# Kernel tuning notes

Hardware: AMD Instinct MI355X
Metric: run time of the kernel (lower is better)

Reference implementation:

```python
import jax, jax.numpy as jnp
import numpy as np

C = 256
NH = 4  # attention heads
G = 8   # groupnorm groups
EPS = 1e-5


def group_norm(x, weight, bias):
    B, Cc, H, W = x.shape
    xg = x.reshape(B, G, Cc // G, H, W)
    mean = xg.mean(axis=(2, 3, 4), keepdims=True)
    var = xg.var(axis=(2, 3, 4), keepdims=True)
    xg = (xg - mean) * jax.lax.rsqrt(var + EPS)
    xn = xg.reshape(B, Cc, H, W)
    return xn * weight[None, :, None, None] + bias[None, :, None, None]


def setup_inputs() -> dict:
    key = jax.random.key(0)
    ks = jax.random.split(key, 7)
    B, H, W = 16, 32, 32
    x = jax.random.normal(ks[0], (B, C, H, W), dtype=jnp.float32)
    n_weight = jnp.ones((C,), dtype=jnp.float32)
    n_bias = jnp.zeros((C,), dtype=jnp.float32)
    qkv_w = jax.random.normal(ks[1], (3 * C, C), dtype=jnp.float32) * (C ** -0.5)
    qkv_b = jnp.zeros((3 * C,), dtype=jnp.float32)
    p_w = jax.random.normal(ks[2], (C, C), dtype=jnp.float32) * (C ** -0.5)
    p_b = jnp.zeros((C,), dtype=jnp.float32)
    return {"x": x, "n_weight": n_weight, "n_bias": n_bias,
            "qkv_w": qkv_w, "qkv_b": qkv_b, "p_w": p_w, "p_b": p_b}


def reference(x, n_weight, n_bias, qkv_w, qkv_b, p_w, p_b):
    B, Cc, H, W = x.shape
    N = H * W
    dh = Cc // NH
    sc = dh ** -0.5
    xn = group_norm(x, n_weight, n_bias)  # [B,C,H,W]
    xn_flat = xn.reshape(B, Cc, N)
    # 1x1 conv == channel matmul
    qkv = jnp.einsum('oc,bcn->bon', qkv_w, xn_flat) + qkv_b[None, :, None]
    qkv = qkv.reshape(B, 3, NH, dh, N)
    q, k, v = qkv[:, 0], qkv[:, 1], qkv[:, 2]  # [B,h,dh,N]
    a = jax.nn.softmax(jnp.einsum('bhci,bhcj->bhij', q, k) * sc, axis=-1)
    o = jnp.einsum('bhij,bhcj->bhci', a, v).reshape(B, Cc, N)
    proj = jnp.einsum('oc,bcn->bon', p_w, o) + p_b[None, :, None]
    return x + proj.reshape(B, Cc, H, W)
```

## Files before the change

kernel.cpp:

```cpp
#include <hip/hip_runtime.h>
#include <math.h>

typedef unsigned short ushort;
typedef unsigned int uint;
typedef __attribute__((ext_vector_type(8))) short bf16x8;
typedef __attribute__((ext_vector_type(4))) float f32x4;

constexpr int Bc  = 16;
constexpr float EPSc = 1e-5f;
constexpr float QSC  = 0.18033688f;

__device__ inline ushort f2bf(float f) {
    uint u = __float_as_uint(f);
    uint r = (u + 0x7fffu + ((u >> 16) & 1u)) >> 16;
    return (ushort)r;
}
__device__ inline uint pack2(float a, float b) {
    return (uint)f2bf(a) | ((uint)f2bf(b) << 16);
}
__device__ __forceinline__ uint cvt2(float a, float b) {
#if __has_builtin(__builtin_amdgcn_cvt_pk_bf16_f32)
    auto v = __builtin_amdgcn_cvt_pk_bf16_f32(a, b);
    uint u; __builtin_memcpy(&u, &v, 4); return u;
#else
    return pack2(a, b);
#endif
}
#if __has_builtin(__builtin_amdgcn_exp2f)
#define EXP2F(x) __builtin_amdgcn_exp2f(x)
#else
#define EXP2F(x) __expf((x) * 0.69314718f)
#endif
__device__ __forceinline__ void gl_lds16(const ushort* g, ushort* l) {
    __builtin_amdgcn_global_load_lds(
        (const __attribute__((address_space(1))) void*)g,
        (__attribute__((address_space(3))) void*)l, 16, 0, 0);
}

__global__ __launch_bounds__(256) void pre_k(
    const float* __restrict__ x, const float* __restrict__ qkvw,
    const float* __restrict__ pw, float* __restrict__ pstats,
    ushort* __restrict__ wqb, ushort* __restrict__ pwb) {
    int blk = blockIdx.x;
    if (blk < 512) {
        int bg = blk >> 2, part = blk & 3;
        const float4* p = (const float4*)(x + (size_t)bg * 32768 + part * 8192);
        float s = 0.f, s2 = 0.f;
        for (int i = threadIdx.x; i < 2048; i += 256) {
            float4 v = p[i];
            s += v.x + v.y + v.z + v.w;
            s2 += v.x*v.x + v.y*v.y + v.z*v.z + v.w*v.w;
        }
        __shared__ float rs[256], rq[256];
        rs[threadIdx.x] = s; rq[threadIdx.x] = s2;
        __syncthreads();
        for (int off = 128; off > 0; off >>= 1) {
            if (threadIdx.x < (unsigned)off) {
                rs[threadIdx.x] += rs[threadIdx.x + off];
                rq[threadIdx.x] += rq[threadIdx.x + off];
            }
            __syncthreads();
        }
        if (threadIdx.x == 0) {
            pstats[blk * 2]     = rs[0];
            pstats[blk * 2 + 1] = rq[0];
        }
    } else {
        int idx = ((blk - 512) * 256 + threadIdx.x) * 4;
        if (idx < 196608) {
            int row = idx >> 8;
            float sc = (row < 256) ? QSC : 1.f;
            float4 v = *(const float4*)&qkvw[idx];
            uint2 u; u.x = pack2(v.x * sc, v.y * sc); u.y = pack2(v.z * sc, v.w * sc);
            *(uint2*)&wqb[idx] = u;
        } else {
            int j = idx - 196608;
            float4 v = *(const float4*)&pw[j];
            uint2 u; u.x = pack2(v.x, v.y); u.y = pack2(v.z, v.w);
            *(uint2*)&pwb[j] = u;
        }
    }
}

__global__ __launch_bounds__(256) void norm_t_k(
    const float* __restrict__ x, const float* __restrict__ pstats,
    const float* __restrict__ nw, const float* __restrict__ nb,
    ushort* __restrict__ xt) {
    int b = blockIdx.z, ct = blockIdx.y, nt = blockIdx.x;
    __shared__ ushort T[64 * 72];
    int t = threadIdx.x;
    int nn4 = (t & 15) * 4;
#pragma unroll
    for (int p = 0; p < 4; ++p) {
        int cl = (t >> 4) + p * 16;
        int c = ct * 64 + cl;
        int g = c >> 5;
        int base = (b * 8 + g) * 8;
        float s  = (pstats[base] + pstats[base+2]) + (pstats[base+4] + pstats[base+6]);
        float s2 = (pstats[base+1] + pstats[base+3]) + (pstats[base+5] + pstats[base+7]);
        float inv_n = 1.f / 32768.f;
        float mean = s * inv_n;
        float var  = s2 * inv_n - mean * mean;
        float inv  = rsqrtf(var + EPSc);
        float sw = inv * nw[c];
        float sb = nb[c] - mean * sw;
        float4 v = *(const float4*)&x[((size_t)(b * 256 + c)) * 1024 + nt * 64 + nn4];
        T[(nn4 + 0) * 72 + cl] = f2bf(v.x * sw + sb);
        T[(nn4 + 1) * 72 + cl] = f2bf(v.y * sw + sb);
        T[(nn4 + 2) * 72 + cl] = f2bf(v.z * sw + sb);
        T[(nn4 + 3) * 72 + cl] = f2bf(v.w * sw + sb);
    }
    __syncthreads();
#pragma unroll
    for (int p = 0; p < 4; ++p) {
        int nn = (t >> 4) + p * 16;
        int c4 = (t & 15) * 4;
        uint2 w = *(const uint2*)&T[nn * 72 + c4];
        *(uint2*)&xt[((size_t)b * 1024 + nt * 64 + nn) * 256 + ct * 64 + c4] = w;
    }
}

__global__ __launch_bounds__(256, 3) void qkv_gemm_k(
    const ushort* __restrict__ wq, const ushort* __restrict__ xt,
    const float* __restrict__ wb, ushort* __restrict__ qkT,
    ushort* __restrict__ vbuf) {
    int b = blockIdx.z, cy = blockIdx.y, sx = blockIdx.x;
    __shared__ ushort POOL[4 * 64 * 72];
    int t = threadIdx.x, lane = t & 63, w = t >> 6;
    int quad = lane >> 4, l15 = lane & 15;
    int wm = w >> 1, wn = w & 1;
    const ushort* wrow = wq + (size_t)cy * 128 * 256;
    const ushort* xrow = xt + ((size_t)b * 1024 + sx * 128) * 256;
    bool tpath = (cy < 4);
    int r0 = t >> 2;
    int cs = (t & 3) ^ (r0 & 3);
    int dst = t * 8;
#pragma unroll
    for (int p = 0; p < 2; ++p) {
        int r = r0 + p * 64;
        gl_lds16(&wrow[(size_t)r * 256 + cs * 8], &POOL[p * 2048 + dst]);
        gl_lds16(&xrow[(size_t)r * 256 + cs * 8], &POOL[4096 + p * 2048 + dst]);
    }
    __syncthreads();
    int p0 = quad ^ (l15 & 3);
    f32x4 acc[4][4] = {};
    int cur = 0;
    for (int ki = 0; ki < 8; ++ki) {
        if (ki < 7) {
            int k0 = (ki + 1) * 32, nx = cur ^ 1;
#pragma unroll
            for (int p = 0; p < 2; ++p) {
                int r = r0 + p * 64;
                gl_lds16(&wrow[(size_t)r * 256 + k0 + cs * 8], &POOL[nx * 8192 + p * 2048 + dst]);
                gl_lds16(&xrow[(size_t)r * 256 + k0 + cs * 8], &POOL[nx * 8192 + 4096 + p * 2048 + dst]);
            }
        }
        const ushort* Wc = &POOL[cur * 8192];
        const ushort* Xc = &POOL[cur * 8192 + 4096];
        const ushort* Am = tpath ? Xc : Wc;
        const ushort* Bn = tpath ? Wc : Xc;
        bf16x8 fa[4], fb[4];
#pragma unroll
        for (int mi = 0; mi < 4; ++mi)
            fa[mi] = *(const bf16x8*)&Am[(wm * 64 + mi * 16 + l15) * 32 + p0 * 8];
#pragma unroll
        for (int ni = 0; ni < 4; ++ni)
            fb[ni] = *(const bf16x8*)&Bn[(wn * 64 + ni * 16 + l15) * 32 + p0 * 8];
#pragma unroll
        for (int mi = 0; mi < 4; ++mi)
#pragma unroll
            for (int ni = 0; ni < 4; ++ni)
                acc[mi][ni] = __builtin_amdgcn_mfma_f32_16x16x32_bf16(
                    fa[mi], fb[ni], acc[mi][ni], 0, 0, 0);
        __syncthreads();
        cur ^= 1;
    }
    ushort* Tw = POOL + w * (64 * 72);
    float bsc = (tpath && cy < 2) ? QSC : 1.f;
    if (tpath) {
#pragma unroll
        for (int ni = 0; ni < 4; ++ni) {
            float bias = wb[cy * 128 + wn * 64 + ni * 16 + l15] * bsc;
#pragma unroll
            for (int mi = 0; mi < 4; ++mi)
#pragma unroll
                for (int rr = 0; rr < 4; ++rr)
                    Tw[(mi * 16 + quad * 4 + rr) * 72 + ni * 16 + l15] =
                        f2bf(acc[mi][ni][rr] + bias);
        }
    } else {
#pragma unroll
        for (int mi = 0; mi < 4; ++mi)
#pragma unroll
            for (int rr = 0; rr < 4; ++rr) {
                float bias = wb[cy * 128 + wm * 64 + mi * 16 + quad * 4 + rr];
#pragma unroll
                for (int ni = 0; ni < 4; ++ni)
                    Tw[(mi * 16 + quad * 4 + rr) * 72 + ni * 16 + l15] =
                        f2bf(acc[mi][ni][rr] + bias);
            }
    }
    __asm__ __volatile__("" ::: "memory");
    int row8 = lane >> 3, ch = lane & 7;
#pragma unroll
    for (int p = 0; p < 8; ++p) {
        int row = p * 8 + row8;
        uint4 u = *(const uint4*)&Tw[row * 72 + ch * 8];
        if (tpath) {
            int sp = sx * 128 + wm * 64 + row;
            *(uint4*)&qkT[((size_t)b * 1024 + sp) * 512 + cy * 128 + wn * 64 + ch * 8] = u;
        } else {
            int chanloc = (cy - 4) * 128 + wm * 64 + row;
            *(uint4*)&vbuf[((size_t)b * 256 + chanloc) * 1024 + sx * 128 + wn * 64 + ch * 8] = u;
        }
    }
}

__global__ __launch_bounds__(256, 3) void attn_k(
    const ushort* __restrict__ qkT, const ushort* __restrict__ vbuf,
    ushort* __restrict__ ot) {
    int i0 = blockIdx.x * 128;
    int bh = blockIdx.y;
    int b = bh >> 2, h = bh & 3;
    const ushort* qTb = qkT + (size_t)b * 1024 * 512 + h * 64;
    const ushort* kTb = qTb + 256;
    const ushort* vb  = vbuf + ((size_t)(b * 256 + h * 64)) * 1024;
    __shared__ ushort Ks[2][4096], Vs[2][4096];
    __shared__ ushort Ps[8 * 1152];
    __shared__ float  Lx[128];
    int t = threadIdx.x, lane = t & 63, w = t >> 6;
    int quad = lane >> 4, l15 = lane & 15;
    bf16x8 aq[2][2];
#pragma unroll
    for (int rb = 0; rb < 2; ++rb) {
        const ushort* qr = &qTb[(size_t)(i0 + rb * 64 + w * 16 + l15) * 512];
        aq[rb][0] = *(const bf16x8*)&qr[quad * 8];
        aq[rb][1] = *(const bf16x8*)&qr[32 + quad * 8];
    }
    int r0 = t >> 3;
    int cs = (t & 7) ^ (r0 & 7);
    int p0 = quad ^ (l15 & 7);
    int p1 = p0 ^ 4;
    gl_lds16(&kTb[(size_t)r0 * 512 + cs * 8],        &Ks[0][t * 8]);
    gl_lds16(&kTb[(size_t)(r0 + 32) * 512 + cs * 8], &Ks[0][t * 8 + 2048]);
    gl_lds16(&vb[(size_t)r0 * 1024 + cs * 8],        &Vs[0][t * 8]);
    gl_lds16(&vb[(size_t)(r0 + 32) * 1024 + cs * 8], &Vs[0][t * 8 + 2048]);
    __syncthreads();
    float lsum0 = 0.f, lsum1 = 0.f;
    f32x4 oacc[2][4] = {};
    ushort* Pw0 = &Ps[(w * 2 + 0) * 1152];
    ushort* Pw1 = &Ps[(w * 2 + 1) * 1152];
    int cur = 0;
    for (int j0 = 0; j0 < 1024; j0 += 64) {
        if (j0 < 960) {
            int jn = j0 + 64, nx = cur ^ 1;
            gl_lds16(&kTb[(size_t)(jn + r0) * 512 + cs * 8],        &Ks[nx][t * 8]);
            gl_lds16(&kTb[(size_t)(jn + r0 + 32) * 512 + cs * 8],   &Ks[nx][t * 8 + 2048]);
            gl_lds16(&vb[(size_t)r0 * 1024 + jn + cs * 8],          &Vs[nx][t * 8]);
            gl_lds16(&vb[(size_t)(r0 + 32) * 1024 + jn + cs * 8],   &Vs[nx][t * 8 + 2048]);
        }
        const ushort* Kc = Ks[cur];
        const ushort* Vc = Vs[cur];
        f32x4 s0[4], s1[4];
#pragma unroll
        for (int jt = 0; jt < 4; ++jt) {
            int row = jt * 16 + l15;
            bf16x8 bk0 = *(const bf16x8*)&Kc[row * 64 + p0 * 8];
            bf16x8 bk1 = *(const bf16x8*)&Kc[row * 64 + p1 * 8];
            f32x4 a = {0.f, 0.f, 0.f, 0.f};
            a = __builtin_amdgcn_mfma_f32_16x16x32_bf16(bk0, aq[0][0], a, 0, 0, 0);
            a = __builtin_amdgcn_mfma_f32_16x16x32_bf16(bk1, aq[0][1], a, 0, 0, 0);
            s0[jt] = a;
            f32x4 c = {0.f, 0.f, 0.f, 0.f};
            c = __builtin_amdgcn_mfma_f32_16x16x32_bf16(bk0, aq[1][0], c, 0, 0, 0);
            c = __builtin_amdgcn_mfma_f32_16x16x32_bf16(bk1, aq[1][1], c, 0, 0, 0);
            s1[jt] = c;
        }
#pragma unroll
        for (int jt = 0; jt < 4; ++jt) {
            int o = l15 * 72 + jt * 16 + quad * 4;
            float e0 = EXP2F(s0[jt][0]), e1 = EXP2F(s0[jt][1]);
            float e2 = EXP2F(s0[jt][2]), e3 = EXP2F(s0[jt][3]);
            lsum0 += (e0 + e1) + (e2 + e3);
            *(uint*)&Pw0[o]     = cvt2(e0, e1);
            *(uint*)&Pw0[o + 2] = cvt2(e2, e3);
            float f0 = EXP2F(s1[jt][0]), f1 = EXP2F(s1[jt][1]);
            float f2 = EXP2F(s1[jt][2]), f3 = EXP2F(s1[jt][3]);
            lsum1 += (f0 + f1) + (f2 + f3);
            *(uint*)&Pw1[o]     = cvt2(f0, f1);
            *(uint*)&Pw1[o + 2] = cvt2(f2, f3);
        }
        __asm__ __volatile__("" ::: "memory");
        bf16x8 ap00 = *(const bf16x8*)&Pw0[l15 * 72 + quad * 8];
        bf16x8 ap01 = *(const bf16x8*)&Pw0[l15 * 72 + 32 + quad * 8];
        bf16x8 ap10 = *(const bf16x8*)&Pw1[l15 * 72 + quad * 8];
        bf16x8 ap11 = *(const bf16x8*)&Pw1[l15 * 72 + 32 + quad * 8];
#pragma unroll
        for (int ct = 0; ct < 4; ++ct) {
            int row = ct * 16 + l15;
            bf16x8 bv0 = *(const bf16x8*)&Vc[row * 64 + p0 * 8];
            bf16x8 bv1 = *(const bf16x8*)&Vc[row * 64 + p1 * 8];
            oacc[0][ct] = __builtin_amdgcn_mfma_f32_16x16x32_bf16(ap00, bv0, oacc[0][ct], 0, 0, 0);
            oacc[0][ct] = __builtin_amdgcn_mfma_f32_16x16x32_bf16(ap01, bv1, oacc[0][ct], 0, 0, 0);
            oacc[1][ct] = __builtin_amdgcn_mfma_f32_16x16x32_bf16(ap10, bv0, oacc[1][ct], 0, 0, 0);
            oacc[1][ct] = __builtin_amdgcn_mfma_f32_16x16x32_bf16(ap11, bv1, oacc[1][ct], 0, 0, 0);
        }
        __syncthreads();
        cur ^= 1;
    }
    lsum0 += __shfl_xor(lsum0, 16); lsum0 += __shfl_xor(lsum0, 32);
    lsum1 += __shfl_xor(lsum1, 16); lsum1 += __shfl_xor(lsum1, 32);
    if (quad == 0) {
        Lx[w * 16 + l15]      = lsum0;
        Lx[64 + w * 16 + l15] = lsum1;
    }
    __asm__ __volatile__("" ::: "memory");
#pragma unroll
    for (int rb = 0; rb < 2; ++rb) {
        float4 lv = *(const float4*)&Lx[rb * 64 + w * 16 + quad * 4];
        float linv[4] = {1.f / lv.x, 1.f / lv.y, 1.f / lv.z, 1.f / lv.w};
        ushort* Pw = (rb == 0) ? Pw0 : Pw1;
#pragma unroll
        for (int ct = 0; ct < 4; ++ct)
#pragma unroll
            for (int rr = 0; rr < 4; ++rr)
                Pw[(quad * 4 + rr) * 72 + ct * 16 + l15] = f2bf(oacc[rb][ct][rr] * linv[rr]);
        __asm__ __volatile__("" ::: "memory");
#pragma unroll
        for (int p = 0; p < 2; ++p) {
            int row = p * 8 + (lane >> 3), ch = lane & 7;
            uint4 u = *(const uint4*)&Pw[row * 72 + ch * 8];
            *(uint4*)&ot[((size_t)b * 1024 + i0 + rb * 64 + w * 16 + row) * 256 + h * 64 + ch * 8] = u;
        }
    }
}

__global__ __launch_bounds__(256, 3) void proj_k(
    const ushort* __restrict__ pwb, const ushort* __restrict__ ot,
    const float* __restrict__ pb, const float* __restrict__ x,
    float* __restrict__ out) {
    int b = blockIdx.z, cy = blockIdx.y, sx = blockIdx.x;
    __shared__ ushort SB[2][2][128 * 32];
    int t = threadIdx.x, lane = t & 63, w = t >> 6;
    int quad = lane >> 4, l15 = lane & 15;
    int wm = w >> 1, wn = w & 1;
    const ushort* wrow = pwb + (size_t)cy * 128 * 256;
    const ushort* xrow = ot + ((size_t)b * 1024 + sx * 128) * 256;
    int r0 = t >> 2;
    int cs = (t & 3) ^ (r0 & 3);
    int dst = t * 8;
#pragma unroll
    for (int p = 0; p < 2; ++p) {
        int r = r0 + p * 64;
        gl_lds16(&wrow[(size_t)r * 256 + cs * 8], &SB[0][0][p * 2048 + dst]);
        gl_lds16(&xrow[(size_t)r * 256 + cs * 8], &SB[0][1][p * 2048 + dst]);
    }
    __syncthreads();
    int p0 = quad ^ (l15 & 3);
    f32x4 acc[4][4] = {};
    int cur = 0;
    for (int ki = 0; ki < 8; ++ki) {
        if (ki < 7) {
            int k0 = (ki + 1) * 32, nx = cur ^ 1;
#pragma unroll
            for (int p = 0; p < 2; ++p) {
                int r = r0 + p * 64;
                gl_lds16(&wrow[(size_t)r * 256 + k0 + cs * 8], &SB[nx][0][p * 2048 + dst]);
                gl_lds16(&xrow[(size_t)r * 256 + k0 + cs * 8], &SB[nx][1][p * 2048 + dst]);
            }
        }
        const ushort* Wc = SB[cur][0];
        const ushort* Xc = SB[cur][1];
        bf16x8 fa[4], fb[4];
#pragma unroll
        for (int mi = 0; mi < 4; ++mi)
            fa[mi] = *(const bf16x8*)&Wc[(wm * 64 + mi * 16 + l15) * 32 + p0 * 8];
#pragma unroll
        for (int ni = 0; ni < 4; ++ni)
            fb[ni] = *(const bf16x8*)&Xc[(wn * 64 + ni * 16 + l15) * 32 + p0 * 8];
#pragma unroll
        for (int mi = 0; mi < 4; ++mi)
#pragma unroll
            for (int ni = 0; ni < 4; ++ni)
                acc[mi][ni] = __builtin_amdgcn_mfma_f32_16x16x32_bf16(
                    fa[mi], fb[ni], acc[mi][ni], 0, 0, 0);
        __syncthreads();
        cur ^= 1;
    }
#pragma unroll
    for (int mi = 0; mi < 4; ++mi)
#pragma unroll
        for (int rr = 0; rr < 4; ++rr) {
            int chan = cy * 128 + wm * 64 + mi * 16 + quad * 4 + rr;
            float bias = pb[chan];
#pragma unroll
            for (int ni = 0; ni < 4; ++ni) {
                int sp = sx * 128 + wn * 64 + ni * 16 + l15;
                size_t o = ((size_t)(b * 256 + chan)) * 1024 + sp;
                out[o] = acc[mi][ni][rr] + bias + x[o];
            }
        }
}

extern "C" void kernel_launch(void* const* d_in, const int* in_sizes, int n_in,
                              void* d_out, int out_size, void* d_ws, size_t ws_size,
                              hipStream_t stream) {
    const float* x    = (const float*)d_in[0];
    const float* nw   = (const float*)d_in[1];
    const float* nb   = (const float*)d_in[2];
    const float* qkvw = (const float*)d_in[3];
    const float* qkvb = (const float*)d_in[4];
    const float* pw   = (const float*)d_in[5];
    const float* pb   = (const float*)d_in[6];
    float* out = (float*)d_out;

    float* pstats = (float*)d_ws;
    ushort* base = (ushort*)((char*)d_ws + 4096);
    ushort* xt   = base;
    ushort* wqb  = xt + (size_t)16 * 1024 * 256;
    ushort* pwb  = wqb + 768 * 256;
    ushort* qkT  = pwb + 256 * 256;
    ushort* vbuf = qkT + (size_t)16 * 1024 * 512;
    ushort* ot   = xt;

    pre_k<<<dim3(768), dim3(256), 0, stream>>>(x, qkvw, pw, pstats, wqb, pwb);
    norm_t_k<<<dim3(16, 4, Bc), dim3(256), 0, stream>>>(x, pstats, nw, nb, xt);
    qkv_gemm_k<<<dim3(8, 6, Bc), dim3(256), 0, stream>>>(wqb, xt, qkvb, qkT, vbuf);
    attn_k<<<dim3(8, 64), dim3(256), 0, stream>>>(qkT, vbuf, ot);
    proj_k<<<dim3(8, 2, Bc), dim3(256), 0, stream>>>(pwb, ot, pb, x, out);
}
```

Measured before the change: 138.7 us.

## Replace LDS-staged double buffering with direct global fragment loads in GEMMs and attention

Drops the global_load_lds double-buffered shared-memory staging in the QKV GEMM, attention and projection kernels. MFMA operand fragments are now read straight from global memory (relying on L1/L2), and the per-iteration __syncthreads go away. This cuts LDS traffic and barriers but makes every wave re-fetch K/V and weight tiles from cache. It also loses the software prefetch that overlapped loads with MFMA work.

```diff
diff --git a/kernel.cpp b/kernel.cpp
--- a/kernel.cpp
+++ b/kernel.cpp
@@ -31,11 +31,6 @@
 #else
 #define EXP2F(x) __expf((x) * 0.69314718f)
 #endif
-__device__ __forceinline__ void gl_lds16(const ushort* g, ushort* l) {
-    __builtin_amdgcn_global_load_lds(
-        (const __attribute__((address_space(1))) void*)g,
-        (__attribute__((address_space(3))) void*)l, 16, 0, 0);
-}
 
 __global__ __launch_bounds__(256) void pre_k(
     const float* __restrict__ x, const float* __restrict__ qkvw,
@@ -129,51 +124,28 @@
     int t = threadIdx.x, lane = t & 63, w = t >> 6;
     int quad = lane >> 4, l15 = lane & 15;
     int wm = w >> 1, wn = w & 1;
+    bool tpath = (cy < 4);
     const ushort* wrow = wq + (size_t)cy * 128 * 256;
     const ushort* xrow = xt + ((size_t)b * 1024 + sx * 128) * 256;
-    bool tpath = (cy < 4);
-    int r0 = t >> 2;
-    int cs = (t & 3) ^ (r0 & 3);
-    int dst = t * 8;
-#pragma unroll
-    for (int p = 0; p < 2; ++p) {
-        int r = r0 + p * 64;
-        gl_lds16(&wrow[(size_t)r * 256 + cs * 8], &POOL[p * 2048 + dst]);
-        gl_lds16(&xrow[(size_t)r * 256 + cs * 8], &POOL[4096 + p * 2048 + dst]);
-    }
-    __syncthreads();
-    int p0 = quad ^ (l15 & 3);
+    const ushort* arow = tpath ? xrow : wrow;
+    const ushort* brow = tpath ? wrow : xrow;
     f32x4 acc[4][4] = {};
-    int cur = 0;
-    for (int ki = 0; ki < 8; ++ki) {
-        if (ki < 7) {
-            int k0 = (ki + 1) * 32, nx = cur ^ 1;
-#pragma unroll
-            for (int p = 0; p < 2; ++p) {
-                int r = r0 + p * 64;
-                gl_lds16(&wrow[(size_t)r * 256 + k0 + cs * 8], &POOL[nx * 8192 + p * 2048 + dst]);
-                gl_lds16(&xrow[(size_t)r * 256 + k0 + cs * 8], &POOL[nx * 8192 + 4096 + p * 2048 + dst]);
-            }
-        }
-        const ushort* Wc = &POOL[cur * 8192];
-        const ushort* Xc = &POOL[cur * 8192 + 4096];
-        const ushort* Am = tpath ? Xc : Wc;
-        const ushort* Bn = tpath ? Wc : Xc;
+#pragma unroll 2
+    for (int ks = 0; ks < 8; ++ks) {
+        int k0 = ks * 32 + quad * 8;
         bf16x8 fa[4], fb[4];
 #pragma unroll
         for (int mi = 0; mi < 4; ++mi)
-            fa[mi] = *(const bf16x8*)&Am[(wm * 64 + mi * 16 + l15) * 32 + p0 * 8];
+            fa[mi] = *(const bf16x8*)&arow[(size_t)(wm * 64 + mi * 16 + l15) * 256 + k0];
 #pragma unroll
         for (int ni = 0; ni < 4; ++ni)
-            fb[ni] = *(const bf16x8*)&Bn[(wn * 64 + ni * 16 + l15) * 32 + p0 * 8];
+            fb[ni] = *(const bf16x8*)&brow[(size_t)(wn * 64 + ni * 16 + l15) * 256 + k0];
 #pragma unroll
         for (int mi = 0; mi < 4; ++mi)
 #pragma unroll
             for (int ni = 0; ni < 4; ++ni)
                 acc[mi][ni] = __builtin_amdgcn_mfma_f32_16x16x32_bf16(
                     fa[mi], fb[ni], acc[mi][ni], 0, 0, 0);
-        __syncthreads();
-        cur ^= 1;
     }
     ushort* Tw = POOL + w * (64 * 72);
     float bsc = (tpath && cy < 2) ? QSC : 1.f;
@@ -225,7 +197,6 @@
     const ushort* qTb = qkT + (size_t)b * 1024 * 512 + h * 64;
     const ushort* kTb = qTb + 256;
     const ushort* vb  = vbuf + ((size_t)(b * 256 + h * 64)) * 1024;
-    __shared__ ushort Ks[2][4096], Vs[2][4096];
     __shared__ ushort Ps[8 * 1152];
     __shared__ float  Lx[128];
     int t = threadIdx.x, lane = t & 63, w = t >> 6;
@@ -237,36 +208,17 @@
         aq[rb][0] = *(const bf16x8*)&qr[quad * 8];
         aq[rb][1] = *(const bf16x8*)&qr[32 + quad * 8];
     }
-    int r0 = t >> 3;
-    int cs = (t & 7) ^ (r0 & 7);
-    int p0 = quad ^ (l15 & 7);
-    int p1 = p0 ^ 4;
-    gl_lds16(&kTb[(size_t)r0 * 512 + cs * 8],        &Ks[0][t * 8]);
-    gl_lds16(&kTb[(size_t)(r0 + 32) * 512 + cs * 8], &Ks[0][t * 8 + 2048]);
-    gl_lds16(&vb[(size_t)r0 * 1024 + cs * 8],        &Vs[0][t * 8]);
-    gl_lds16(&vb[(size_t)(r0 + 32) * 1024 + cs * 8], &Vs[0][t * 8 + 2048]);
-    __syncthreads();
     float lsum0 = 0.f, lsum1 = 0.f;
     f32x4 oacc[2][4] = {};
     ushort* Pw0 = &Ps[(w * 2 + 0) * 1152];
     ushort* Pw1 = &Ps[(w * 2 + 1) * 1152];
-    int cur = 0;
     for (int j0 = 0; j0 < 1024; j0 += 64) {
-        if (j0 < 960) {
-            int jn = j0 + 64, nx = cur ^ 1;
-            gl_lds16(&kTb[(size_t)(jn + r0) * 512 + cs * 8],        &Ks[nx][t * 8]);
-            gl_lds16(&kTb[(size_t)(jn + r0 + 32) * 512 + cs * 8],   &Ks[nx][t * 8 + 2048]);
-            gl_lds16(&vb[(size_t)r0 * 1024 + jn + cs * 8],          &Vs[nx][t * 8]);
-            gl_lds16(&vb[(size_t)(r0 + 32) * 1024 + jn + cs * 8],   &Vs[nx][t * 8 + 2048]);
-        }
-        const ushort* Kc = Ks[cur];
-        const ushort* Vc = Vs[cur];
         f32x4 s0[4], s1[4];
 #pragma unroll
         for (int jt = 0; jt < 4; ++jt) {
-            int row = jt * 16 + l15;
-            bf16x8 bk0 = *(const bf16x8*)&Kc[row * 64 + p0 * 8];
-            bf16x8 bk1 = *(const bf16x8*)&Kc[row * 64 + p1 * 8];
+            const ushort* kr = &kTb[(size_t)(j0 + jt * 16 + l15) * 512];
+            bf16x8 bk0 = *(const bf16x8*)&kr[quad * 8];
+            bf16x8 bk1 = *(const bf16x8*)&kr[32 + quad * 8];
             f32x4 a = {0.f, 0.f, 0.f, 0.f};
             a = __builtin_amdgcn_mfma_f32_16x16x32_bf16(bk0, aq[0][0], a, 0, 0, 0);
             a = __builtin_amdgcn_mfma_f32_16x16x32_bf16(bk1, aq[0][1], a, 0, 0, 0);
@@ -297,16 +249,14 @@
         bf16x8 ap11 = *(const bf16x8*)&Pw1[l15 * 72 + 32 + quad * 8];
 #pragma unroll
         for (int ct = 0; ct < 4; ++ct) {
-            int row = ct * 16 + l15;
-            bf16x8 bv0 = *(const bf16x8*)&Vc[row * 64 + p0 * 8];
-            bf16x8 bv1 = *(const bf16x8*)&Vc[row * 64 + p1 * 8];
+            const ushort* vr = &vb[(size_t)(ct * 16 + l15) * 1024 + j0];
+            bf16x8 bv0 = *(const bf16x8*)&vr[quad * 8];
+            bf16x8 bv1 = *(const bf16x8*)&vr[32 + quad * 8];
             oacc[0][ct] = __builtin_amdgcn_mfma_f32_16x16x32_bf16(ap00, bv0, oacc[0][ct], 0, 0, 0);
             oacc[0][ct] = __builtin_amdgcn_mfma_f32_16x16x32_bf16(ap01, bv1, oacc[0][ct], 0, 0, 0);
             oacc[1][ct] = __builtin_amdgcn_mfma_f32_16x16x32_bf16(ap10, bv0, oacc[1][ct], 0, 0, 0);
             oacc[1][ct] = __builtin_amdgcn_mfma_f32_16x16x32_bf16(ap11, bv1, oacc[1][ct], 0, 0, 0);
         }
-        __syncthreads();
-        cur ^= 1;
     }
     lsum0 += __shfl_xor(lsum0, 16); lsum0 += __shfl_xor(lsum0, 32);
     lsum1 += __shfl_xor(lsum1, 16); lsum1 += __shfl_xor(lsum1, 32);
@@ -340,52 +290,28 @@
     const float* __restrict__ pb, const float* __restrict__ x,
     float* __restrict__ out) {
     int b = blockIdx.z, cy = blockIdx.y, sx = blockIdx.x;
-    __shared__ ushort SB[2][2][128 * 32];
     int t = threadIdx.x, lane = t & 63, w = t >> 6;
     int quad = lane >> 4, l15 = lane & 15;
     int wm = w >> 1, wn = w & 1;
     const ushort* wrow = pwb + (size_t)cy * 128 * 256;
     const ushort* xrow = ot + ((size_t)b * 1024 + sx * 128) * 256;
-    int r0 = t >> 2;
-    int cs = (t & 3) ^ (r0 & 3);
-    int dst = t * 8;
-#pragma unroll
-    for (int p = 0; p < 2; ++p) {
-        int r = r0 + p * 64;
-        gl_lds16(&wrow[(size_t)r * 256 + cs * 8], &SB[0][0][p * 2048 + dst]);
-        gl_lds16(&xrow[(size_t)r * 256 + cs * 8], &SB[0][1][p * 2048 + dst]);
-    }
-    __syncthreads();
-    int p0 = quad ^ (l15 & 3);
     f32x4 acc[4][4] = {};
-    int cur = 0;
-    for (int ki = 0; ki < 8; ++ki) {
-        if (ki < 7) {
-            int k0 = (ki + 1) * 32, nx = cur ^ 1;
-#pragma unroll
-            for (int p = 0; p < 2; ++p) {
-                int r = r0 + p * 64;
-                gl_lds16(&wrow[(size_t)r * 256 + k0 + cs * 8], &SB[nx][0][p * 2048 + dst]);
-                gl_lds16(&xrow[(size_t)r * 256 + k0 + cs * 8], &SB[nx][1][p * 2048 + dst]);
-            }
-        }
-        const ushort* Wc = SB[cur][0];
-        const ushort* Xc = SB[cur][1];
+#pragma unroll 2
+    for (int ks = 0; ks < 8; ++ks) {
+        int k0 = ks * 32 + quad * 8;
         bf16x8 fa[4], fb[4];
 #pragma unroll
         for (int mi = 0; mi < 4; ++mi)
-            fa[mi] = *(const bf16x8*)&Wc[(wm * 64 + mi * 16 + l15) * 32 + p0 * 8];
+            fa[mi] = *(const bf16x8*)&wrow[(size_t)(wm * 64 + mi * 16 + l15) * 256 + k0];
 #pragma unroll
         for (int ni = 0; ni < 4; ++ni)
-            fb[ni] = *(const bf16x8*)&Xc[(wn * 64 + ni * 16 + l15) * 32 + p0 * 8];
+            fb[ni] = *(const bf16x8*)&xrow[(size_t)(wn * 64 + ni * 16 + l15) * 256 + k0];
 #pragma unroll
         for (int mi = 0; mi < 4; ++mi)
 #pragma unroll
             for (int ni = 0; ni < 4; ++ni)
                 acc[mi][ni] = __builtin_amdgcn_mfma_f32_16x16x32_bf16(
                     fa[mi], fb[ni], acc[mi][ni], 0, 0, 0);
-        __syncthreads();
-        cur ^= 1;
     }
 #pragma unroll
     for (int mi = 0; mi < 4; ++mi)
```

Result: slower. 198.8 us (+43.3%).
